# Kernel optimization log

Measured on AMD Instinct MI355X. Metric: run time of the kernel, lower is better.

Reference implementation:

```python
import jax, jax.numpy as jnp
import numpy as np
from math import factorial

# ---- configuration (init_kwargs: nclasses=40, cfg.bw=16) ----
BW = 16            # spherical bandwidth
NB = 2 * BW        # grid samples per angle
M = 2 * BW - 1     # spectral orders m in [-(BW-1), BW-1]
OFF = BW - 1       # index offset: m -> m + OFF
NCLS = 40
EPS = 1e-5
BATCH = 8

_FACT = [float(factorial(i)) for i in range(4 * BW + 2)]

def _wigner_d(l, beta):
    """Wigner small-d matrix d^l_{m',m}(beta), shape [2l+1, 2l+1]."""
    c, s = np.cos(beta / 2.0), np.sin(beta / 2.0)
    d = np.zeros((2 * l + 1, 2 * l + 1))
    for imp, mp in enumerate(range(-l, l + 1)):
        for im, m in enumerate(range(-l, l + 1)):
            pref = np.sqrt(_FACT[l + mp] * _FACT[l - mp] * _FACT[l + m] * _FACT[l - m])
            acc = 0.0
            for k in range(max(0, m - mp), min(l + m, l - mp) + 1):
                acc += ((-1.0) ** (mp - m + k)
                        / (_FACT[l + m - k] * _FACT[k] * _FACT[l - k - mp] * _FACT[k - m + mp])
                        * c ** (2 * l - 2 * k + m - mp) * s ** (2 * k - m + mp))
            d[imp, im] = pref * acc
    return d

def _build_constants():
    # Driscoll-Healy beta quadrature grid and weights
    betas = np.pi * (2 * np.arange(NB) + 1) / (4 * BW)
    kk = np.arange(BW)
    qw = (2.0 / BW) * np.sin(betas) * (
        np.sin(np.outer(2 * np.arange(NB) + 1, 2 * kk + 1) * np.pi / (4 * BW)) @ (1.0 / (2 * kk + 1)))
    d_beta = np.zeros((NB, BW, M, M))      # d^l_{mn}(beta_j), zero-padded over l
    for j, beta in enumerate(betas):
        for l in range(BW):
            d_beta[j, l, OFF - l:OFF + l + 1, OFF - l:OFF + l + 1] = _wigner_d(l, beta)
    d_eq = np.zeros((BW, M, M))            # d^l_{mn}(pi/2) for the equatorial kernel grid
    for l in range(BW):
        d_eq[l, OFF - l:OFF + l + 1, OFF - l:OFF + l + 1] = _wigner_d(l, np.pi / 2)
    bins = (np.arange(-(BW - 1), BW) % NB).astype(np.int32)  # FFT bin for each order m
    return qw.astype(np.float32), d_beta.astype(np.float32), d_eq.astype(np.float32), bins

_QWn, _DBETAn, _DEQn, _BINSn = _build_constants()
_DBJ = jnp.asarray(_DBETAn)                                   # [NB, L, M, M]
_DEQJ = jnp.asarray(_DEQn)                                    # [L, M, M]
_DEQ0 = jnp.asarray(_DEQn[:, :, OFF])                         # [L, M]  (n = 0 column)
_WD_S2 = jnp.asarray(_QWn[:, None, None] * _DBETAn[:, :, :, OFF])   # [NB, L, M]
_WD_SO3 = jnp.asarray(_QWn[:, None, None, None] * _DBETAn)          # [NB, L, M, M]
_L2 = jnp.asarray((2.0 * np.arange(BW) + 1.0).astype(np.float32))
_BINSJ = jnp.asarray(_BINSn)

def _so3_ifft(z, bias):
    # z: [B, Co, L, M, M] SO(3) spectrum -> real signal [B, Co, NB(beta), NB(alpha), NB(gamma)]
    F = jnp.einsum('bolmn,jlmn,l->bojmn', z, _DBJ, _L2)
    grid = jnp.zeros(F.shape[:3] + (NB, NB), F.dtype)
    grid = grid.at[..., _BINSJ[:, None], _BINSJ[None, :]].set(F)
    sig = jnp.fft.ifft2(grid, axes=(-2, -1)).real * float(NB * NB)
    return sig + bias[None, :, None, None, None]

def _s2_conv(x, W, bias):
    # x: [B, Ci, NB(beta), NB(alpha)]; W: [Ci, Co, NB] kernel on the equatorial grid
    Xf = jnp.fft.fft(x, axis=-1)[..., _BINSJ]                 # [B,Ci,NB,M]
    xh = jnp.einsum('bcjm,jlm->bclm', Xf, _WD_S2)             # S2 FFT -> [B,Ci,L,M]
    Wf = jnp.fft.fft(W, axis=-1)[..., _BINSJ]                 # [Ci,Co,M]
    yh = _DEQ0[:, :, None, None] * jnp.transpose(Wf, (2, 0, 1))[None]   # [L,N,Ci,Co]
    z = jnp.einsum('bilm,lnio->bolmn', xh, jnp.conj(yh))      # S2 correlation -> SO(3) spectrum
    return _so3_ifft(z, bias)

def _so3_conv(x, W, bias):
    # x: [B, Ci, NB(beta), NB(alpha), NB(gamma)]; W: [Ci, Co, NB]
    Xf = jnp.fft.fft2(x, axes=(-2, -1))[..., _BINSJ[:, None], _BINSJ[None, :]]  # [B,Ci,NB,M,M]
    xh = jnp.einsum('bcjmn,jlmn->bclmn', Xf, _WD_SO3)         # SO(3) FFT -> [B,Ci,L,M,M]
    Wf = jnp.fft.fft(W, axis=-1)[..., _BINSJ]                 # [Ci,Co,M]
    yh = _DEQJ[:, :, :, None, None] * jnp.transpose(Wf, (2, 0, 1))[None, :, None]  # [L,N,K,Ci,Co]
    z = jnp.einsum('bilmk,lnkio->bolmn', xh, jnp.conj(yh))    # SO(3) correlation
    return _so3_ifft(z, bias)

def _bn(h, g, b, axes, shape):
    mu = jnp.mean(h, axes, keepdims=True)
    var = jnp.var(h, axes, keepdims=True)
    return (h - mu) * jax.lax.rsqrt(var + EPS) * g.reshape(shape) + b.reshape(shape)

def _forward(x, k1, c1b, bn1_g, bn1_b, k2, c2b, bn2_g, bn2_b, k3, c3b, bn3_g, bn3_b,
             fc1_w, fc1_b, fbn1_g, fbn1_b, fc2_w, fc2_b, fbn2_g, fbn2_b, fc3_w, fc3_b):
    s5 = (1, -1, 1, 1, 1)
    h = _s2_conv(x, k1, c1b)                                  # [B,50,NB,NB,NB]
    h = jax.nn.relu(_bn(h, bn1_g, bn1_b, (0, 2, 3, 4), s5))
    h = _so3_conv(h, k2, c2b)
    h = jax.nn.relu(_bn(h, bn2_g, bn2_b, (0, 2, 3, 4), s5))
    h = _so3_conv(h, k3, c3b)
    h = jax.nn.relu(_bn(h, bn3_g, bn3_b, (0, 2, 3, 4), s5))
    h = h.mean(-1)                                            # integrate over gamma
    h = h.reshape(h.shape[0], h.shape[1], -1).max(-1)         # global max pool -> [B,50]
    h = h @ fc1_w.T + fc1_b
    h = jax.nn.relu(_bn(h, fbn1_g, fbn1_b, (0,), (1, -1)))
    h = h @ fc2_w.T + fc2_b
    h = jax.nn.relu(_bn(h, fbn2_g, fbn2_b, (0,), (1, -1)))
    h = h @ fc3_w.T + fc3_b
    return jax.nn.log_softmax(h, axis=1)

def setup_inputs():
    key = jax.random.key(0)
    ks = jax.random.split(key, 24)
    f32 = jnp.float32
    def kern(k, ci, co):
        return jax.random.normal(k, (ci, co, NB), f32) / np.sqrt(ci * NB).astype(np.float32)
    def lin(k, co, ci):
        return jax.random.normal(k, (co, ci), f32) / np.sqrt(ci).astype(np.float32)
    return {
        'x': jax.random.normal(ks[0], (BATCH, 1, NB, NB), f32),
        'k1': kern(ks[1], 1, 50), 'c1b': 0.01 * jax.random.normal(ks[2], (50,), f32),
        'bn1_g': 1.0 + 0.1 * jax.random.normal(ks[3], (50,), f32),
        'bn1_b': 0.1 * jax.random.normal(ks[4], (50,), f32),
        'k2': kern(ks[5], 50, 50), 'c2b': 0.01 * jax.random.normal(ks[6], (50,), f32),
        'bn2_g': 1.0 + 0.1 * jax.random.normal(ks[7], (50,), f32),
        'bn2_b': 0.1 * jax.random.normal(ks[8], (50,), f32),
        'k3': kern(ks[9], 50, 50), 'c3b': 0.01 * jax.random.normal(ks[10], (50,), f32),
        'bn3_g': 1.0 + 0.1 * jax.random.normal(ks[11], (50,), f32),
        'bn3_b': 0.1 * jax.random.normal(ks[12], (50,), f32),
        'fc1_w': lin(ks[13], 256, 50), 'fc1_b': jnp.zeros((256,), f32),
        'fbn1_g': 1.0 + 0.1 * jax.random.normal(ks[14], (256,), f32),
        'fbn1_b': 0.1 * jax.random.normal(ks[15], (256,), f32),
        'fc2_w': lin(ks[16], 128, 256), 'fc2_b': jnp.zeros((128,), f32),
        'fbn2_g': 1.0 + 0.1 * jax.random.normal(ks[17], (128,), f32),
        'fbn2_b': 0.1 * jax.random.normal(ks[18], (128,), f32),
        'fc3_w': lin(ks[19], NCLS, 128), 'fc3_b': jnp.zeros((NCLS,), f32),
    }

def reference(x, k1, c1b, bn1_g, bn1_b, k2, c2b, bn2_g, bn2_b, k3, c3b, bn3_g, bn3_b,
              fc1_w, fc1_b, fbn1_g, fbn1_b, fc2_w, fc2_b, fbn2_g, fbn2_b, fc3_w, fc3_b):
    return _forward(x, k1, c1b, bn1_g, bn1_b, k2, c2b, bn2_g, bn2_b, k3, c3b, bn3_g, bn3_b,
                    fc1_w, fc1_b, fbn1_g, fbn1_b, fc2_w, fc2_b, fbn2_g, fbn2_b, fc3_w, fc3_b)
```

## Files before the change

### kernel.cpp

```cpp
#include <hip/hip_runtime.h>
#include <math.h>

constexpr int NB = 32;
constexpr int LL = 16;
constexpr int MM = 31;
constexpr int MOFF = 15;
constexpr int NBATCH = 8;
constexpr int NCH = 50;
constexpr int NQ = MM * MM;
constexpr int SPAT = NB * NB * NB;
constexpr long long HN = (long long)NBATCH * NCH * SPAT;

#define PI_D 3.14159265358979323846

__device__ inline float2 c_mk(float x, float y) { float2 r; r.x = x; r.y = y; return r; }

__device__ inline void fill_tw(float2* tw) {
  int t = threadIdx.x;
  if (t < 32) {
    double a = (double)t * (PI_D / 16.0);
    tw[t] = c_mk((float)cos(a), (float)sin(a));
  }
}

__device__ inline int bitrev5(int n) {
  return ((n & 1) << 4) | ((n & 2) << 2) | (n & 4) | ((n & 8) >> 2) | ((n & 16) >> 4);
}

__device__ inline double dpow(double x, int n) {
  double r = 1.0;
  for (int i = 0; i < n; ++i) r *= x;
  return r;
}


__global__ void qw_kernel(float* __restrict__ qw) {
  int j = threadIdx.x;
  if (j >= NB) return;
  double beta = PI_D * (2 * j + 1) / 64.0;
  double acc = 0.0;
  for (int kk = 0; kk < LL; ++kk)
    acc += sin((double)(2 * j + 1) * (2 * kk + 1) * PI_D / 64.0) / (double)(2 * kk + 1);
  qw[j] = (float)((2.0 / 16.0) * sin(beta) * acc);
}

__global__ void wigner_kernel(float* __restrict__ out, int nj, int eqmode) {
  __shared__ double fact[66];
  int tid = threadIdx.x;
  if (tid < 66) { double f = 1.0; for (int i = 2; i <= tid; ++i) f *= (double)i; fact[tid] = f; }
  __syncthreads();
  int total = nj * LL * NQ;
  int idx = blockIdx.x * blockDim.x + tid;
  if (idx >= total) return;
  int q = idx % NQ;
  int l = (idx / NQ) % LL;
  int j = idx / (NQ * LL);
  int mp = q / MM - MOFF;
  int m  = q % MM - MOFF;
  int amp = mp < 0 ? -mp : mp, am = m < 0 ? -m : m;
  float res = 0.f;
  if (amp <= l && am <= l) {
    double beta = eqmode ? (PI_D * 0.5) : (PI_D * (2 * j + 1) / 64.0);
    double c = cos(beta * 0.5), s = sin(beta * 0.5);
    double pref = sqrt(fact[l + mp] * fact[l - mp] * fact[l + m] * fact[l - m]);
    int k0 = max(0, m - mp), k1 = min(l + m, l - mp);
    double acc = 0.0;
    for (int k = k0; k <= k1; ++k) {
      double denom = fact[l + m - k] * fact[k] * fact[l - k - mp] * fact[k - m + mp];
      double term = dpow(c, 2 * l - 2 * k + m - mp) * dpow(s, 2 * k - m + mp) / denom;
      acc += ((mp - m + k) & 1) ? -term : term;
    }
    res = (float)(pref * acc);
  }
  out[idx] = res;
}

__global__ void transpose_d_kernel(const float* __restrict__ dbeta, float* __restrict__ dbT) {
  int idx = blockIdx.x * blockDim.x + threadIdx.x;
  if (idx >= NB * LL * NQ) return;
  int m = idx % MM;
  int n = (idx / MM) % MM;
  int jl = idx / NQ;
  dbT[idx] = dbeta[jl * NQ + m * MM + n];
}


__global__ __launch_bounds__(256) void s2_xh_kernel(const float* __restrict__ x,
                                                    const float* __restrict__ qw,
                                                    const float* __restrict__ dbeta,
                                                    float2* __restrict__ xh1) {
  __shared__ float xt[NB * NB];
  __shared__ float2 Xf0[NB * MM];
  __shared__ float2 tw[32];
  fill_tw(tw);
  int tid = threadIdx.x, b = blockIdx.x;
  for (int e = tid; e < NB * NB; e += 256) xt[e] = x[b * 1024 + e];
  __syncthreads();
  for (int e = tid; e < NB * MM; e += 256) {
    int j = e / MM, mi = e % MM, m = mi - MOFF;
    float re = 0.f, im = 0.f;
    const float* row = xt + j * NB;
    for (int a = 0; a < NB; ++a) {
      float v = row[a];
      float2 t = tw[(m * a) & 31];
      re += v * t.x; im -= v * t.y;
    }
    Xf0[e] = c_mk(re, im);
  }
  __syncthreads();
  for (int e = tid; e < LL * MM; e += 256) {
    int l = e / MM, mi = e % MM;
    float re = 0.f, im = 0.f;
    for (int j = 0; j < NB; ++j) {
      float w = qw[j] * dbeta[(j * LL + l) * NQ + mi * MM + MOFF];
      float2 X = Xf0[j * MM + mi];
      re += w * X.x; im += w * X.y;
    }
    xh1[(b * LL + l) * MM + mi] = c_mk(re, im);
  }
}

__global__ __launch_bounds__(256) void wfft_kernel(const float* __restrict__ W, int CiCo,
                                                   float2* __restrict__ Wf) {
  __shared__ float2 tw[32];
  fill_tw(tw);
  __syncthreads();
  int idx = blockIdx.x * blockDim.x + threadIdx.x;
  if (idx >= MM * CiCo) return;
  int ni = idx / CiCo, ic = idx % CiCo;
  int n = ni - MOFF;
  float re = 0.f, im = 0.f;
  for (int t = 0; t < NB; ++t) {
    float v = W[ic * NB + t];
    float2 tt = tw[(n * t) & 31];
    re += v * tt.x; im -= v * tt.y;
  }
  Wf[idx] = c_mk(re, im);
}

__global__ void s2_z_kernel(const float2* __restrict__ xh1, const float2* __restrict__ Wf1,
                            const float* __restrict__ deq, float2* __restrict__ z) {
  int idx = blockIdx.x * blockDim.x + threadIdx.x;
  if (idx >= NBATCH * NCH * LL * NQ) return;
  int mi = idx % MM; int t = idx / MM;
  int ni = t % MM; t /= MM;
  int l = t % LL; t /= LL;
  int o = t % NCH; int b = t / NCH;
  float d0 = deq[(l * MM + ni) * MM + MOFF];
  float2 xv = xh1[(b * LL + l) * MM + mi];
  float2 wv = Wf1[ni * NCH + o];
  float re = d0 * (xv.x * wv.x + xv.y * wv.y);
  float im = d0 * (xv.y * wv.x - xv.x * wv.y);
  z[idx] = c_mk(re, im);
}


__global__ __launch_bounds__(256) void fjq_kernel(const float2* __restrict__ z,
                                                  const float* __restrict__ dbT,
                                                  float2* __restrict__ F) {
  __shared__ float2 zs[2][LL][8];
  int qg = blockIdx.x % 121;
  int bg = blockIdx.x / 121;
  int tid = threadIdx.x;
  int j = tid >> 3, ql = tid & 7;
  int q = qg * 8 + ql;
  bool qok = q < NQ;
  int qc = qok ? q : NQ - 1;
  float w[LL];
  #pragma unroll
  for (int l = 0; l < LL; ++l)
    w[l] = (2.f * l + 1.f) * dbT[(j * LL + l) * NQ + qc];
  int bo0 = bg * 25;
  if (tid < 128) {
    int l = tid >> 3, qq = qg * 8 + (tid & 7);
    int dd = (qq < NQ) ? (qq / MM - MOFF) : 99; if (dd < 0) dd = -dd;
    zs[0][l][tid & 7] = (l >= dd) ? z[((long long)bo0 * LL + l) * NQ + qq] : c_mk(0.f, 0.f);
  }
  __syncthreads();
  for (int i = 0; i < 25; ++i) {
    int bo = bo0 + i;
    if (i < 24 && tid < 128) {
      int l = tid >> 3, qq = qg * 8 + (tid & 7);
      int dd = (qq < NQ) ? (qq / MM - MOFF) : 99; if (dd < 0) dd = -dd;
      zs[(i + 1) & 1][l][tid & 7] =
          (l >= dd) ? z[((long long)(bo + 1) * LL + l) * NQ + qq] : c_mk(0.f, 0.f);
    }
    float fr = 0.f, fi = 0.f;
    #pragma unroll
    for (int l = 0; l < LL; ++l) {
      float2 zv = zs[i & 1][l][ql];
      fr += w[l] * zv.x; fi += w[l] * zv.y;
    }
    if (qok) F[((long long)bo * NB + j) * NQ + q] = c_mk(fr, fi);
    __syncthreads();
  }
}

__global__ __launch_bounds__(64) void so3_dft_kernel(const float2* __restrict__ F,
                                                     const float* __restrict__ bias,
                                                     float* __restrict__ out,
                                                     float2* __restrict__ parts) {
  __shared__ float Sre[2][32][33];
  __shared__ float Sim[2][32][33];
  __shared__ float2 tw[32];
  fill_tw(tw);
  int tid = threadIdx.x;
  int lane = tid & 31;
  int t = tid >> 5;
  int idx = blockIdx.x * 2 + t;
  int j = idx & 31;
  int bo = idx >> 5;
  int o = bo % NCH;

  Sre[t][16][lane] = 0.f; Sim[t][16][lane] = 0.f;
  Sre[t][lane][16] = 0.f; Sim[t][lane][16] = 0.f;
  __syncthreads();

  const float2* src = F + ((long long)bo * NB + j) * NQ;
  for (int e = lane; e < NQ; e += 32) {
    int ni = e / MM, mi = e % MM;
    float2 v = src[e];
    Sre[t][(ni + 17) & 31][(mi + 17) & 31] = v.x;
    Sim[t][(ni + 17) & 31][(mi + 17) & 31] = v.y;
  }
  __syncthreads();

  float vr[32], vi[32];

  #pragma unroll
  for (int r = 0; r < 32; ++r) { vr[r] = Sre[t][r][lane]; vi[r] = Sim[t][r][lane]; }
  #pragma unroll
  for (int st = 0; st < 5; ++st) {
    const int half = 16 >> st, tmul = 1 << st;
    #pragma unroll
    for (int p = 0; p < 16; ++p) {
      const int j2 = p & (half - 1);
      const int i0 = ((p >> (4 - st)) << (5 - st)) + j2;
      const int i1 = i0 + half;
      float2 tt = tw[(j2 * tmul) & 31];
      float ur = vr[i0], ui = vi[i0], wr = vr[i1], wi = vi[i1];
      float dr = ur - wr, di = ui - wi;
      vr[i0] = ur + wr; vi[i0] = ui + wi;
      vr[i1] = dr * tt.x - di * tt.y;
      vi[i1] = dr * tt.y + di * tt.x;
    }
  }
  #pragma unroll
  for (int k = 0; k < 32; ++k) {
    Sre[t][k][lane] = vr[bitrev5(k)];
    Sim[t][k][lane] = vi[bitrev5(k)];
  }
  __syncthreads();

  #pragma unroll
  for (int m = 0; m < 32; ++m) { vr[m] = Sre[t][lane][m]; vi[m] = Sim[t][lane][m]; }
  #pragma unroll
  for (int st = 0; st < 5; ++st) {
    const int half = 16 >> st, tmul = 1 << st;
    #pragma unroll
    for (int p = 0; p < 16; ++p) {
      const int j2 = p & (half - 1);
      const int i0 = ((p >> (4 - st)) << (5 - st)) + j2;
      const int i1 = i0 + half;
      float2 tt = tw[(j2 * tmul) & 31];
      float ur = vr[i0], ui = vi[i0], wr = vr[i1], wi = vi[i1];
      float dr = ur - wr, di = ui - wi;
      vr[i0] = ur + wr; vi[i0] = ui + wi;
      vr[i1] = dr * tt.x - di * tt.y;
      vi[i1] = dr * tt.y + di * tt.x;
    }
  }

  float bval = bias[o];
  long long obase = (long long)bo * SPAT + (long long)j * 1024 + lane;
  float s1 = 0.f, s2 = 0.f;
  #pragma unroll
  for (int a = 0; a < 32; ++a) {
    float val = vr[bitrev5(a)] + bval;
    out[obase + a * 32] = val;
    s1 += val; s2 += val * val;
  }
  #pragma unroll
  for (int off = 32; off > 0; off >>= 1) {
    s1 += __shfl_down(s1, off);
    s2 += __shfl_down(s2, off);
  }
  if (tid == 0) {
    atomicAdd(&parts[bo].x, s1);
    atomicAdd(&parts[bo].y, s2);
  }
}


__global__ void bn_finalize_kernel(const float2* __restrict__ partials,
                                   const float* __restrict__ g, const float* __restrict__ bb,
                                   float2* __restrict__ sc) {
  int o = threadIdx.x;
  if (o >= NCH) return;
  float s = 0.f, ss = 0.f;
  for (int b = 0; b < NBATCH; ++b) { float2 p = partials[b * NCH + o]; s += p.x; ss += p.y; }
  float inv = 1.f / (float)(NBATCH * SPAT);
  float mu = s * inv;
  float var = ss * inv - mu * mu;
  float scale = g[o] * rsqrtf(var + 1e-5f);
  sc[o] = c_mk(scale, bb[o] - mu * scale);
}


__global__ __launch_bounds__(256) void dft2b_kernel(const float* __restrict__ h,
                                                    const float2* __restrict__ sc,
                                                    float2* __restrict__ Xf) {
  __shared__ float xt[32 * 33];
  __shared__ float2 P[32 * 16];
  __shared__ float2 Xs[NQ];
  __shared__ float2 tw[32];
  fill_tw(tw);
  int tid = threadIdx.x;
  long long blk = blockIdx.x;
  int c = (int)((blk >> 5) % NCH);
  float2 s = sc[c];
  const float* src = h + blk * 1024;
  for (int e = tid; e < 1024; e += 256) {
    float v = src[e];
    xt[(e >> 5) * 33 + (e & 31)] = fmaxf(v * s.x + s.y, 0.f);
  }
  __syncthreads();
  for (int e = tid; e < 512; e += 256) {
    int a = e >> 4, n = e & 15;
    float re = 0.f, im = 0.f;
    const float* row = xt + a * 33;
    #pragma unroll
    for (int g = 0; g < 32; ++g) {
      float v = row[g];
      float2 t = tw[(n * g) & 31];
      re += v * t.x; im -= v * t.y;
    }
    P[a * 16 + n] = c_mk(re, im);
  }
  __syncthreads();
  {
    int e = tid;
    if (e < 256) {
      int mh = e >> 4, n = e & 15;
      float sxx = 0.f, sxy = 0.f, syx = 0.f, syy = 0.f;
      #pragma unroll
      for (int a = 0; a < 32; ++a) {
        float2 p = P[a * 16 + n];
        float2 t = tw[(mh * a) & 31];
        sxx += p.x * t.x; sxy += p.x * t.y;
        syx += p.y * t.x; syy += p.y * t.y;
      }
      float2 Xp = c_mk(sxx + syy, syx - sxy);
      float2 Xm = c_mk(sxx - syy, syx + sxy);
      Xs[(mh + MOFF) * MM + (n + MOFF)] = Xp;
      Xs[(MOFF - mh) * MM + (n + MOFF)] = Xm;
      Xs[(MOFF - mh) * MM + (MOFF - n)] = c_mk(Xp.x, -Xp.y);
      Xs[(mh + MOFF) * MM + (MOFF - n)] = c_mk(Xm.x, -Xm.y);
    }
  }
  __syncthreads();
  float2* dst = Xf + blk * NQ;
  for (int e = tid; e < NQ; e += 256) dst[e] = Xs[e];
}

__global__ void xh_kernel(const float2* __restrict__ Xf, const float* __restrict__ qw,
                          const float* __restrict__ dbeta, float2* __restrict__ xh) {
  int idx = blockIdx.x * blockDim.x + threadIdx.x;
  if (idx >= NBATCH * NCH * NQ) return;
  int q = idx % NQ;
  int bc = idx / NQ;
  float2 acc[LL];
  #pragma unroll
  for (int l = 0; l < LL; ++l) acc[l] = c_mk(0.f, 0.f);
  for (int j = 0; j < NB; ++j) {
    float2 xv = Xf[((long long)bc * NB + j) * NQ + q];
    float qj = qw[j];
    const float* dbase = dbeta + (long long)(j * LL) * NQ + q;
    #pragma unroll
    for (int l = 0; l < LL; ++l) {
      float w = qj * dbase[l * NQ];
      acc[l].x += w * xv.x;
      acc[l].y += w * xv.y;
    }
  }
  #pragma unroll
  for (int l = 0; l < LL; ++l) xh[((long long)bc * LL + l) * NQ + q] = acc[l];
}

__global__ __launch_bounds__(64) void hk_kernel(const float2* __restrict__ xh,
                                                const float* __restrict__ deq,
                                                float2* __restrict__ hk2) {
  int r = blockIdx.x;
  int mi = r % MM;
  int lb = r / MM;
  int b = lb & 7;
  int l = lb >> 3;
  int adm = mi - MOFF; adm = adm < 0 ? -adm : adm;
  if (adm > l) return;
  int ich = threadIdx.x;
  if (ich >= NCH) return;
  float2 row[MM];
  const float2* src = xh + ((long long)(b * NCH + ich) * LL + l) * NQ + mi * MM;
  #pragma unroll
  for (int k = 0; k < MM; ++k) row[k] = src[k];
  const float* dl = deq + l * NQ;
  long long obase = (long long)r * MM * NCH + ich;
  for (int ni = MOFF - l; ni <= MOFF + l; ++ni) {
    const float* dr = dl + ni * MM;
    float re = 0.f, im = 0.f;
    #pragma unroll
    for (int k = 0; k < MM; ++k) {
      float d = dr[k];
      re += d * row[k].x;
      im += d * row[k].y;
    }
    hk2[obase + (long long)ni * NCH] = c_mk(re, im);
  }
}

__global__ __launch_bounds__(256) void z_kernel(const float2* __restrict__ hk2,
                                                const float2* __restrict__ Wf,
                                                float2* __restrict__ z) {
  __shared__ float2 ws[NCH * NCH];
  int blk = blockIdx.x;
  int ni = 0;
  for (;;) {
    int d = ni - MOFF; if (d < 0) d = -d;
    int nt = 32 - 2 * d;
    if (blk < nt) break;
    blk -= nt; ++ni;
  }
  int dmin = ni - MOFF; if (dmin < 0) dmin = -dmin;
  int tid = threadIdx.x;
  {
    const float4* s4 = reinterpret_cast<const float4*>(Wf + ni * (NCH * NCH));
    float4* d4 = reinterpret_cast<float4*>(ws);
    for (int e = tid; e < NCH * NCH / 2; e += 256) d4[e] = s4[e];
  }
  __syncthreads();
  if (tid >= 248) return;
  int r = dmin * 248 + blk * 124 + (tid % 124);
  int o0 = (tid / 124) * 25;
  int mi = r % MM;
  int rem = r / MM;
  int b = rem & 7;
  int l = rem >> 3;

  const float4* h4 = reinterpret_cast<const float4*>(hk2 + ((long long)r * MM + ni) * NCH);

  float2 acc[25];
  #pragma unroll
  for (int u = 0; u < 25; ++u) acc[u] = c_mk(0.f, 0.f);

  for (int ih = 0; ih < 25; ++ih) {
    float4 hv = h4[ih];
    const float2* w0 = ws + (2 * ih) * NCH + o0;
    #pragma unroll
    for (int u = 0; u < 25; ++u) {
      float2 w = w0[u];
      acc[u].x += hv.x * w.x + hv.y * w.y;
      acc[u].y += hv.y * w.x - hv.x * w.y;
    }
    const float2* w1 = w0 + NCH;
    #pragma unroll
    for (int u = 0; u < 25; ++u) {
      float2 w = w1[u];
      acc[u].x += hv.z * w.x + hv.w * w.y;
      acc[u].y += hv.w * w.x - hv.z * w.y;
    }
  }

  long long zbase = (((long long)(b * NCH + o0) * LL + l) * NQ) + ni * MM + mi;
  #pragma unroll
  for (int u = 0; u < 25; ++u)
    z[zbase + (long long)u * LL * NQ] = acc[u];
}


__global__ void pool_kernel(const float* __restrict__ h, const float2* __restrict__ sc,
                            float* __restrict__ pooled) {
  __shared__ float sm[256];
  int tid = threadIdx.x;
  int o = blockIdx.x % NCH;
  float2 s = sc[o];
  const float* base = h + (long long)blockIdx.x * SPAT;
  float best = -1e30f;
  for (int e = tid; e < 1024; e += 256) {
    float acc = 0.f;
    for (int g = 0; g < NB; ++g) {
      float v = base[e * NB + g];
      acc += fmaxf(v * s.x + s.y, 0.f);
    }
    best = fmaxf(best, acc * (1.f / 32.f));
  }
  sm[tid] = best;
  __syncthreads();
  for (int st = 128; st > 0; st >>= 1) {
    if (tid < st) sm[tid] = fmaxf(sm[tid], sm[tid + st]);
    __syncthreads();
  }
  if (tid == 0) pooled[blockIdx.x] = sm[0];
}

__global__ __launch_bounds__(256) void head_kernel(const float* __restrict__ pooled,
    const float* __restrict__ fc1w, const float* __restrict__ fc1b,
    const float* __restrict__ g1, const float* __restrict__ b1,
    const float* __restrict__ fc2w, const float* __restrict__ fc2b,
    const float* __restrict__ g2, const float* __restrict__ b2,
    const float* __restrict__ fc3w, const float* __restrict__ fc3b,
    float* __restrict__ out) {
  __shared__ float pin[NBATCH * NCH];
  __shared__ float A[NBATCH * 256];
  __shared__ float Bm[NBATCH * 128];
  __shared__ float Cm[NBATCH * 40];
  int tid = threadIdx.x;
  for (int e = tid; e < NBATCH * NCH; e += 256) pin[e] = pooled[e];
  __syncthreads();
  {
    float v[NBATCH];
    #pragma unroll
    for (int b = 0; b < NBATCH; ++b) {
      float acc = fc1b[tid];
      for (int c = 0; c < NCH; ++c) acc += pin[b * NCH + c] * fc1w[tid * NCH + c];
      v[b] = acc;
    }
    float s = 0.f, ss = 0.f;
    #pragma unroll
    for (int b = 0; b < NBATCH; ++b) { s += v[b]; ss += v[b] * v[b]; }
    float mu = s * 0.125f, var = ss * 0.125f - mu * mu;
    float sc = g1[tid] * rsqrtf(var + 1e-5f), sh = b1[tid] - mu * sc;
    #pragma unroll
    for (int b = 0; b < NBATCH; ++b) A[b * 256 + tid] = fmaxf(v[b] * sc + sh, 0.f);
  }
  __syncthreads();
  if (tid < 128) {
    float v[NBATCH];
    #pragma unroll
    for (int b = 0; b < NBATCH; ++b) {
      float acc = fc2b[tid];
      for (int c = 0; c < 256; ++c) acc += A[b * 256 + c] * fc2w[tid * 256 + c];
      v[b] = acc;
    }
    float s = 0.f, ss = 0.f;
    #pragma unroll
    for (int b = 0; b < NBATCH; ++b) { s += v[b]; ss += v[b] * v[b]; }
    float mu = s * 0.125f, var = ss * 0.125f - mu * mu;
    float sc = g2[tid] * rsqrtf(var + 1e-5f), sh = b2[tid] - mu * sc;
    #pragma unroll
    for (int b = 0; b < NBATCH; ++b) Bm[b * 128 + tid] = fmaxf(v[b] * sc + sh, 0.f);
  }
  __syncthreads();
  if (tid < 40) {
    #pragma unroll
    for (int b = 0; b < NBATCH; ++b) {
      float acc = fc3b[tid];
      for (int c = 0; c < 128; ++c) acc += Bm[b * 128 + c] * fc3w[tid * 128 + c];
      Cm[b * 40 + tid] = acc;
    }
  }
  __syncthreads();
  if (tid < NBATCH) {
    int b = tid;
    float mx = -1e30f;
    for (int f = 0; f < 40; ++f) mx = fmaxf(mx, Cm[b * 40 + f]);
    float se = 0.f;
    for (int f = 0; f < 40; ++f) se += expf(Cm[b * 40 + f] - mx);
    float lse = mx + logf(se);
    for (int f = 0; f < 40; ++f) out[b * 40 + f] = Cm[b * 40 + f] - lse;
  }
}


extern "C" void kernel_launch(void* const* d_in, const int* in_sizes, int n_in,
                              void* d_out, int out_size, void* d_ws, size_t ws_size,
                              hipStream_t stream) {
  (void)in_sizes; (void)n_in; (void)out_size;
  const float* x    = (const float*)d_in[0];
  const float* k1   = (const float*)d_in[1];
  const float* c1b  = (const float*)d_in[2];
  const float* bn1g = (const float*)d_in[3];
  const float* bn1b = (const float*)d_in[4];
  const float* k2   = (const float*)d_in[5];
  const float* c2b  = (const float*)d_in[6];
  const float* bn2g = (const float*)d_in[7];
  const float* bn2b = (const float*)d_in[8];
  const float* k3   = (const float*)d_in[9];
  const float* c3b  = (const float*)d_in[10];
  const float* bn3g = (const float*)d_in[11];
  const float* bn3b = (const float*)d_in[12];
  const float* fc1w = (const float*)d_in[13];
  const float* fc1b = (const float*)d_in[14];
  const float* g1   = (const float*)d_in[15];
  const float* bb1  = (const float*)d_in[16];
  const float* fc2w = (const float*)d_in[17];
  const float* fc2b = (const float*)d_in[18];
  const float* g2   = (const float*)d_in[19];
  const float* bb2  = (const float*)d_in[20];
  const float* fc3w = (const float*)d_in[21];
  const float* fc3b = (const float*)d_in[22];
  float* out = (float*)d_out;

  char* ws = (char*)d_ws;
  size_t off = 0;
  auto alloc = [&](size_t n) -> char* {
    char* p = ws + off;
    off += (n + 255) & ~(size_t)255;
    return p;
  };

  float*  dbeta  = (float*)alloc(sizeof(float) * NB * LL * NQ);
  float*  dbT    = (float*)alloc(sizeof(float) * NB * LL * NQ);
  float*  deq    = (float*)alloc(sizeof(float) * LL * NQ);
  float*  qw     = (float*)alloc(sizeof(float) * NB);
  float2* xh1    = (float2*)alloc(sizeof(float2) * NBATCH * LL * MM);
  float2* Wf     = (float2*)alloc(sizeof(float2) * MM * NCH * NCH);
  float2* parts  = (float2*)alloc(sizeof(float2) * NBATCH * NCH);
  float2* bnsc   = (float2*)alloc(sizeof(float2) * 64);
  float*  pooled = (float*)alloc(sizeof(float) * NBATCH * NCH);
  float*  HA     = (float*)alloc(sizeof(float) * (size_t)HN);
  float*  HB     = (float*)alloc(sizeof(float) * (size_t)HN);
  size_t XFB = (size_t)NBATCH * NCH * NB * NQ * sizeof(float2);
  size_t XHB = (size_t)NBATCH * NCH * LL * NQ * sizeof(float2);
  char* AR = alloc(XFB + XHB);
  float2* Xf  = (float2*)AR;
  float2* xh  = (float2*)(AR + XFB);
  float2* hk2 = (float2*)AR;
  float2* zb  = (float2*)(AR + XFB);
  float2* Fb  = (float2*)AR;

  if (ws_size < off) return;

  const int T = 256;
  const size_t PARTS_B = sizeof(float2) * NBATCH * NCH;
  qw_kernel<<<1, 32, 0, stream>>>(qw);
  wigner_kernel<<<(NB * LL * NQ + T - 1) / T, T, 0, stream>>>(dbeta, NB, 0);
  wigner_kernel<<<(LL * NQ + T - 1) / T, T, 0, stream>>>(deq, 1, 1);
  transpose_d_kernel<<<(NB * LL * NQ + T - 1) / T, T, 0, stream>>>(dbeta, dbT);

  s2_xh_kernel<<<NBATCH, T, 0, stream>>>(x, qw, dbeta, xh1);
  wfft_kernel<<<(MM * 1 * NCH + T - 1) / T, T, 0, stream>>>(k1, 1 * NCH, Wf);
  s2_z_kernel<<<(NBATCH * NCH * LL * NQ + T - 1) / T, T, 0, stream>>>(xh1, Wf, deq, zb);
  fjq_kernel<<<121 * 16, T, 0, stream>>>(zb, dbT, Fb);
  hipMemsetAsync(parts, 0, PARTS_B, stream);
  so3_dft_kernel<<<NBATCH * NCH * NB / 2, 64, 0, stream>>>(Fb, c1b, HA, parts);
  bn_finalize_kernel<<<1, 64, 0, stream>>>(parts, bn1g, bn1b, bnsc);

  dft2b_kernel<<<NBATCH * NCH * NB, T, 0, stream>>>(HA, bnsc, Xf);
  xh_kernel<<<(NBATCH * NCH * NQ + T - 1) / T, T, 0, stream>>>(Xf, qw, dbeta, xh);
  wfft_kernel<<<(MM * NCH * NCH + T - 1) / T, T, 0, stream>>>(k2, NCH * NCH, Wf);
  hk_kernel<<<NBATCH * LL * MM, 64, 0, stream>>>(xh, deq, hk2);
  z_kernel<<<512, T, 0, stream>>>(hk2, Wf, zb);
  fjq_kernel<<<121 * 16, T, 0, stream>>>(zb, dbT, Fb);
  hipMemsetAsync(parts, 0, PARTS_B, stream);
  so3_dft_kernel<<<NBATCH * NCH * NB / 2, 64, 0, stream>>>(Fb, c2b, HB, parts);
  bn_finalize_kernel<<<1, 64, 0, stream>>>(parts, bn2g, bn2b, bnsc);

  dft2b_kernel<<<NBATCH * NCH * NB, T, 0, stream>>>(HB, bnsc, Xf);
  xh_kernel<<<(NBATCH * NCH * NQ + T - 1) / T, T, 0, stream>>>(Xf, qw, dbeta, xh);
  wfft_kernel<<<(MM * NCH * NCH + T - 1) / T, T, 0, stream>>>(k3, NCH * NCH, Wf);
  hk_kernel<<<NBATCH * LL * MM, 64, 0, stream>>>(xh, deq, hk2);
  z_kernel<<<512, T, 0, stream>>>(hk2, Wf, zb);
  fjq_kernel<<<121 * 16, T, 0, stream>>>(zb, dbT, Fb);
  hipMemsetAsync(parts, 0, PARTS_B, stream);
  so3_dft_kernel<<<NBATCH * NCH * NB / 2, 64, 0, stream>>>(Fb, c3b, HA, parts);
  bn_finalize_kernel<<<1, 64, 0, stream>>>(parts, bn3g, bn3b, bnsc);

  pool_kernel<<<NBATCH * NCH, T, 0, stream>>>(HA, bnsc, pooled);
  head_kernel<<<1, T, 0, stream>>>(pooled, fc1w, fc1b, g1, bb1,
                                   fc2w, fc2b, g2, bb2, fc3w, fc3b, out);
}
```

Baseline: 799.2 us.

## Stage FC weights in shared memory and skip zero Wigner-degree writes in xh

The head kernel now copies fc1, fc2 (in two 64-row chunks) and fc3 weights into padded shared memory and recomputes the matmuls from there. fc2 uses float4 dot products with all 256 threads, and fc3 splits work across 160 threads instead of 40. The goal is to cut uncoalesced global weight reads and raise thread utilisation in a single-block kernel. Separately, xh_kernel skips storing coefficients for degrees l below max(|m|,|n|), which are structurally zero, to reduce store traffic, provided downstream kernels never read those entries.

```diff
diff --git a/kernel.cpp b/kernel.cpp
--- a/kernel.cpp
+++ b/kernel.cpp
@@ -369,6 +369,9 @@
   if (idx >= NBATCH * NCH * NQ) return;
   int q = idx % NQ;
   int bc = idx / NQ;
+  int dm = q / MM - MOFF; if (dm < 0) dm = -dm;
+  int dn = q % MM - MOFF; if (dn < 0) dn = -dn;
+  int lmin = dm > dn ? dm : dn;
   float2 acc[LL];
   #pragma unroll
   for (int l = 0; l < LL; ++l) acc[l] = c_mk(0.f, 0.f);
@@ -384,7 +387,8 @@
     }
   }
   #pragma unroll
-  for (int l = 0; l < LL; ++l) xh[((long long)bc * LL + l) * NQ + q] = acc[l];
+  for (int l = 0; l < LL; ++l)
+    if (l >= lmin) xh[((long long)bc * LL + l) * NQ + q] = acc[l];
 }
 
 __global__ __launch_bounds__(64) void hk_kernel(const float2* __restrict__ xh,
@@ -509,54 +513,101 @@
     const float* __restrict__ g2, const float* __restrict__ b2,
     const float* __restrict__ fc3w, const float* __restrict__ fc3b,
     float* __restrict__ out) {
+  __shared__ __align__(16) float WB[64 * 260];
   __shared__ float pin[NBATCH * NCH];
   __shared__ float A[NBATCH * 256];
+  __shared__ float R[NBATCH * 128];
   __shared__ float Bm[NBATCH * 128];
   __shared__ float Cm[NBATCH * 40];
   int tid = threadIdx.x;
+
   for (int e = tid; e < NBATCH * NCH; e += 256) pin[e] = pooled[e];
-  __syncthreads();
+  for (int e = tid; e < 256 * 50; e += 256) {
+    int row = e / 50, c = e % 50;
+    WB[row * 51 + c] = fc1w[e];
+  }
+  __syncthreads();
+
   {
+    int o = tid;
+    const float* wr = WB + o * 51;
     float v[NBATCH];
+    float bias = fc1b[o];
     #pragma unroll
     for (int b = 0; b < NBATCH; ++b) {
-      float acc = fc1b[tid];
-      for (int c = 0; c < NCH; ++c) acc += pin[b * NCH + c] * fc1w[tid * NCH + c];
+      float acc = bias;
+      #pragma unroll
+      for (int c = 0; c < NCH; ++c) acc += pin[b * NCH + c] * wr[c];
       v[b] = acc;
     }
     float s = 0.f, ss = 0.f;
     #pragma unroll
     for (int b = 0; b < NBATCH; ++b) { s += v[b]; ss += v[b] * v[b]; }
     float mu = s * 0.125f, var = ss * 0.125f - mu * mu;
-    float sc = g1[tid] * rsqrtf(var + 1e-5f), sh = b1[tid] - mu * sc;
-    #pragma unroll
-    for (int b = 0; b < NBATCH; ++b) A[b * 256 + tid] = fmaxf(v[b] * sc + sh, 0.f);
-  }
-  __syncthreads();
+    float sc = g1[o] * rsqrtf(var + 1e-5f), sh = b1[o] - mu * sc;
+    #pragma unroll
+    for (int b = 0; b < NBATCH; ++b) A[b * 256 + o] = fmaxf(v[b] * sc + sh, 0.f);
+  }
+  __syncthreads();
+
+  for (int ch = 0; ch < 2; ++ch) {
+    {
+      const float4* s4 = reinterpret_cast<const float4*>(fc2w + ch * 64 * 256);
+      float4* d4 = reinterpret_cast<float4*>(WB);
+      for (int e = tid; e < 64 * 64; e += 256) {
+        int row = e >> 6, k = e & 63;
+        d4[row * 65 + k] = s4[e];
+      }
+    }
+    __syncthreads();
+    {
+      int b = tid >> 5, oo = tid & 31;
+      int o_a = ch * 64 + oo, o_b = o_a + 32;
+      float acc0 = fc2b[o_a], acc1 = fc2b[o_b];
+      const float4* av4 = reinterpret_cast<const float4*>(A + b * 256);
+      const float4* w04 = reinterpret_cast<const float4*>(WB + oo * 260);
+      const float4* w14 = reinterpret_cast<const float4*>(WB + (oo + 32) * 260);
+      #pragma unroll
+      for (int c4 = 0; c4 < 64; ++c4) {
+        float4 av = av4[c4];
+        float4 w0 = w04[c4];
+        float4 w1 = w14[c4];
+        acc0 += av.x * w0.x + av.y * w0.y + av.z * w0.z + av.w * w0.w;
+        acc1 += av.x * w1.x + av.y * w1.y + av.z * w1.z + av.w * w1.w;
+      }
+      R[b * 128 + o_a] = acc0;
+      R[b * 128 + o_b] = acc1;
+    }
+    __syncthreads();
+  }
   if (tid < 128) {
-    float v[NBATCH];
-    #pragma unroll
-    for (int b = 0; b < NBATCH; ++b) {
-      float acc = fc2b[tid];
-      for (int c = 0; c < 256; ++c) acc += A[b * 256 + c] * fc2w[tid * 256 + c];
-      v[b] = acc;
-    }
+    int o = tid;
     float s = 0.f, ss = 0.f;
     #pragma unroll
-    for (int b = 0; b < NBATCH; ++b) { s += v[b]; ss += v[b] * v[b]; }
+    for (int b = 0; b < NBATCH; ++b) { float v = R[b * 128 + o]; s += v; ss += v * v; }
     float mu = s * 0.125f, var = ss * 0.125f - mu * mu;
-    float sc = g2[tid] * rsqrtf(var + 1e-5f), sh = b2[tid] - mu * sc;
-    #pragma unroll
-    for (int b = 0; b < NBATCH; ++b) Bm[b * 128 + tid] = fmaxf(v[b] * sc + sh, 0.f);
-  }
-  __syncthreads();
-  if (tid < 40) {
-    #pragma unroll
-    for (int b = 0; b < NBATCH; ++b) {
-      float acc = fc3b[tid];
-      for (int c = 0; c < 128; ++c) acc += Bm[b * 128 + c] * fc3w[tid * 128 + c];
-      Cm[b * 40 + tid] = acc;
-    }
+    float sc = g2[o] * rsqrtf(var + 1e-5f), sh = b2[o] - mu * sc;
+    #pragma unroll
+    for (int b = 0; b < NBATCH; ++b) Bm[b * 128 + o] = fmaxf(R[b * 128 + o] * sc + sh, 0.f);
+  }
+  for (int e = tid; e < 40 * 128; e += 256) {
+    int row = e >> 7, c = e & 127;
+    WB[row * 129 + c] = fc3w[e];
+  }
+  __syncthreads();
+
+  if (tid < 160) {
+    int o = tid >> 2, q = tid & 3;
+    const float* wr = WB + o * 129;
+    float a0 = fc3b[o], a1 = a0;
+    #pragma unroll
+    for (int c = 0; c < 128; ++c) {
+      float w = wr[c];
+      a0 += Bm[q * 128 + c] * w;
+      a1 += Bm[(q + 4) * 128 + c] * w;
+    }
+    Cm[q * 40 + o] = a0;
+    Cm[(q + 4) * 40 + o] = a1;
   }
   __syncthreads();
   if (tid < NBATCH) {
```

Result: faster. 782.2 us (-2.1%).

## Fuse pooling and MLP head via last-block atomic counter; skip invalid xh stores

Applied to the files above, without the earlier changes.

Merges pool and head kernels into one launch where the last finishing block, detected with an atomic counter, runs the MLP head. The head now stages fc1/fc2/fc3 weights in padded shared memory with coalesced loads and float4 dot products instead of strided global reads. xh_kernel also skips writes for l below max(|m|,|n|). The large shared-memory footprint lowers occupancy of the pooling phase, and correctness now relies on a counter reset and on downstream kernels not reading the skipped entries.

```diff
diff --git a/kernel.cpp b/kernel.cpp
--- a/kernel.cpp
+++ b/kernel.cpp
@@ -369,6 +369,9 @@
   if (idx >= NBATCH * NCH * NQ) return;
   int q = idx % NQ;
   int bc = idx / NQ;
+  int dm = q / MM - MOFF; if (dm < 0) dm = -dm;
+  int dn = q % MM - MOFF; if (dn < 0) dn = -dn;
+  int lmin = dm > dn ? dm : dn;
   float2 acc[LL];
   #pragma unroll
   for (int l = 0; l < LL; ++l) acc[l] = c_mk(0.f, 0.f);
@@ -384,7 +387,8 @@
     }
   }
   #pragma unroll
-  for (int l = 0; l < LL; ++l) xh[((long long)bc * LL + l) * NQ + q] = acc[l];
+  for (int l = 0; l < LL; ++l)
+    if (l >= lmin) xh[((long long)bc * LL + l) * NQ + q] = acc[l];
 }
 
 __global__ __launch_bounds__(64) void hk_kernel(const float2* __restrict__ xh,
@@ -476,87 +480,192 @@
     z[zbase + (long long)u * LL * NQ] = acc[u];
 }
 
-
-__global__ void pool_kernel(const float* __restrict__ h, const float2* __restrict__ sc,
-                            float* __restrict__ pooled) {
-  __shared__ float sm[256];
-  int tid = threadIdx.x;
-  int o = blockIdx.x % NCH;
-  float2 s = sc[o];
-  const float* base = h + (long long)blockIdx.x * SPAT;
-  float best = -1e30f;
-  for (int e = tid; e < 1024; e += 256) {
-    float acc = 0.f;
-    for (int g = 0; g < NB; ++g) {
-      float v = base[e * NB + g];
-      acc += fmaxf(v * s.x + s.y, 0.f);
-    }
-    best = fmaxf(best, acc * (1.f / 32.f));
-  }
-  sm[tid] = best;
-  __syncthreads();
-  for (int st = 128; st > 0; st >>= 1) {
-    if (tid < st) sm[tid] = fmaxf(sm[tid], sm[tid + st]);
-    __syncthreads();
-  }
-  if (tid == 0) pooled[blockIdx.x] = sm[0];
-}
-
-__global__ __launch_bounds__(256) void head_kernel(const float* __restrict__ pooled,
+__global__ __launch_bounds__(256) void pool_head_kernel(const float* __restrict__ h,
+    const float2* __restrict__ sc, float* __restrict__ pooled, unsigned* __restrict__ counter,
     const float* __restrict__ fc1w, const float* __restrict__ fc1b,
     const float* __restrict__ g1, const float* __restrict__ b1,
     const float* __restrict__ fc2w, const float* __restrict__ fc2b,
     const float* __restrict__ g2, const float* __restrict__ b2,
     const float* __restrict__ fc3w, const float* __restrict__ fc3b,
     float* __restrict__ out) {
-  __shared__ float pin[NBATCH * NCH];
-  __shared__ float A[NBATCH * 256];
-  __shared__ float Bm[NBATCH * 128];
-  __shared__ float Cm[NBATCH * 40];
+  __shared__ float sm[256];
+  __shared__ int lastflag;
+  __shared__ __align__(16) float  WB2[12800];
+  __shared__ __align__(16) float4 WB1[2][32 * 65];
+  __shared__ float pin[400];
+  __shared__ __align__(16) float A[8 * 256];
+  __shared__ float R[8 * 128];
+  __shared__ float Cm[8 * 40];
+
   int tid = threadIdx.x;
-  for (int e = tid; e < NBATCH * NCH; e += 256) pin[e] = pooled[e];
-  __syncthreads();
+  int bo = blockIdx.x;
   {
+    int o = bo % NCH;
+    float2 s = sc[o];
+    const float* base = h + (long long)bo * SPAT;
+    float best = -1e30f;
+    for (int e = tid; e < 1024; e += 256) {
+      float acc = 0.f;
+      for (int g = 0; g < NB; ++g) {
+        float v = base[e * NB + g];
+        acc += fmaxf(v * s.x + s.y, 0.f);
+      }
+      best = fmaxf(best, acc * (1.f / 32.f));
+    }
+    sm[tid] = best;
+    __syncthreads();
+    for (int st = 128; st > 0; st >>= 1) {
+      if (tid < st) sm[tid] = fmaxf(sm[tid], sm[tid + st]);
+      __syncthreads();
+    }
+    if (tid == 0) {
+      __hip_atomic_store(&pooled[bo], sm[0], __ATOMIC_RELEASE, __HIP_MEMORY_SCOPE_AGENT);
+      unsigned prev = __hip_atomic_fetch_add(counter, 1u, __ATOMIC_ACQ_REL,
+                                             __HIP_MEMORY_SCOPE_AGENT);
+      lastflag = (prev == 399u);
+    }
+    __syncthreads();
+    if (!lastflag) return;
+  }
+
+  for (int e = tid; e < 400; e += 256)
+    pin[e] = __hip_atomic_load(&pooled[e], __ATOMIC_RELAXED, __HIP_MEMORY_SCOPE_AGENT);
+  #pragma unroll
+  for (int k = 0; k < 50; ++k) WB2[k * 256 + tid] = fc1w[k * 256 + tid];
+  const float4* w2src = reinterpret_cast<const float4*>(fc2w);
+  #pragma unroll
+  for (int k = 0; k < 8; ++k) {
+    int idx = k * 256 + tid;
+    WB1[0][(idx >> 6) * 65 + (idx & 63)] = w2src[idx];
+  }
+  #pragma unroll
+  for (int k = 0; k < 8; ++k) {
+    int idx = k * 256 + tid;
+    WB1[1][(idx >> 6) * 65 + (idx & 63)] = w2src[2048 + idx];
+  }
+  float4 p2r[8], p3r[8];
+  #pragma unroll
+  for (int k = 0; k < 8; ++k) p2r[k] = w2src[4096 + k * 256 + tid];
+  #pragma unroll
+  for (int k = 0; k < 8; ++k) p3r[k] = w2src[6144 + k * 256 + tid];
+  float f3r[20];
+  #pragma unroll
+  for (int k = 0; k < 20; ++k) f3r[k] = fc3w[k * 256 + tid];
+  float rb1 = fc1b[tid], rg1 = g1[tid], rbb1 = b1[tid];
+  int oo = tid & 31, bb = tid >> 5;
+  float f2b[4];
+  #pragma unroll
+  for (int p = 0; p < 4; ++p) f2b[p] = fc2b[p * 32 + oo];
+  float rg2 = 0.f, rbb2 = 0.f;
+  if (tid < 128) { rg2 = g2[tid]; rbb2 = b2[tid]; }
+  float rb3 = (tid < 160) ? fc3b[tid >> 2] : 0.f;
+  __syncthreads();
+
+  {
+    const float* wr = WB2 + tid * 50;
     float v[NBATCH];
     #pragma unroll
-    for (int b = 0; b < NBATCH; ++b) {
-      float acc = fc1b[tid];
-      for (int c = 0; c < NCH; ++c) acc += pin[b * NCH + c] * fc1w[tid * NCH + c];
-      v[b] = acc;
+    for (int b = 0; b < NBATCH; ++b) v[b] = rb1;
+    for (int c = 0; c < NCH; ++c) {
+      float w = wr[c];
+      #pragma unroll
+      for (int b = 0; b < NBATCH; ++b) v[b] += pin[b * NCH + c] * w;
     }
     float s = 0.f, ss = 0.f;
     #pragma unroll
     for (int b = 0; b < NBATCH; ++b) { s += v[b]; ss += v[b] * v[b]; }
     float mu = s * 0.125f, var = ss * 0.125f - mu * mu;
-    float sc = g1[tid] * rsqrtf(var + 1e-5f), sh = b1[tid] - mu * sc;
-    #pragma unroll
-    for (int b = 0; b < NBATCH; ++b) A[b * 256 + tid] = fmaxf(v[b] * sc + sh, 0.f);
-  }
-  __syncthreads();
+    float scl = rg1 * rsqrtf(var + 1e-5f), sh = rbb1 - mu * scl;
+    #pragma unroll
+    for (int b = 0; b < NBATCH; ++b) A[b * 256 + tid] = fmaxf(v[b] * scl + sh, 0.f);
+  }
+  __syncthreads();
+  #pragma unroll
+  for (int k = 0; k < 20; ++k) {
+    int e = k * 256 + tid;
+    WB2[(e >> 7) * 129 + (e & 127)] = f3r[k];
+  }
+
+  const float4* av4 = reinterpret_cast<const float4*>(A) + bb * 64;
+  {
+    const float4* w4 = &WB1[0][oo * 65];
+    float acc = f2b[0];
+    #pragma unroll
+    for (int c4 = 0; c4 < 64; ++c4) {
+      float4 a = av4[c4], w = w4[c4];
+      acc += a.x * w.x + a.y * w.y + a.z * w.z + a.w * w.w;
+    }
+    R[bb * 128 + oo] = acc;
+  }
+  __syncthreads();
+  #pragma unroll
+  for (int k = 0; k < 8; ++k) {
+    int idx = k * 256 + tid;
+    WB1[0][(idx >> 6) * 65 + (idx & 63)] = p2r[k];
+  }
+  {
+    const float4* w4 = &WB1[1][oo * 65];
+    float acc = f2b[1];
+    #pragma unroll
+    for (int c4 = 0; c4 < 64; ++c4) {
+      float4 a = av4[c4], w = w4[c4];
+      acc += a.x * w.x + a.y * w.y + a.z * w.z + a.w * w.w;
+    }
+    R[bb * 128 + 32 + oo] = acc;
+  }
+  __syncthreads();
+  #pragma unroll
+  for (int k = 0; k < 8; ++k) {
+    int idx = k * 256 + tid;
+    WB1[1][(idx >> 6) * 65 + (idx & 63)] = p3r[k];
+  }
+  {
+    const float4* w4 = &WB1[0][oo * 65];
+    float acc = f2b[2];
+    #pragma unroll
+    for (int c4 = 0; c4 < 64; ++c4) {
+      float4 a = av4[c4], w = w4[c4];
+      acc += a.x * w.x + a.y * w.y + a.z * w.z + a.w * w.w;
+    }
+    R[bb * 128 + 64 + oo] = acc;
+  }
+  __syncthreads();
+  {
+    const float4* w4 = &WB1[1][oo * 65];
+    float acc = f2b[3];
+    #pragma unroll
+    for (int c4 = 0; c4 < 64; ++c4) {
+      float4 a = av4[c4], w = w4[c4];
+      acc += a.x * w.x + a.y * w.y + a.z * w.z + a.w * w.w;
+    }
+    R[bb * 128 + 96 + oo] = acc;
+  }
+  __syncthreads();
+
   if (tid < 128) {
-    float v[NBATCH];
-    #pragma unroll
-    for (int b = 0; b < NBATCH; ++b) {
-      float acc = fc2b[tid];
-      for (int c = 0; c < 256; ++c) acc += A[b * 256 + c] * fc2w[tid * 256 + c];
-      v[b] = acc;
-    }
     float s = 0.f, ss = 0.f;
     #pragma unroll
-    for (int b = 0; b < NBATCH; ++b) { s += v[b]; ss += v[b] * v[b]; }
+    for (int b = 0; b < NBATCH; ++b) { float v = R[b * 128 + tid]; s += v; ss += v * v; }
     float mu = s * 0.125f, var = ss * 0.125f - mu * mu;
-    float sc = g2[tid] * rsqrtf(var + 1e-5f), sh = b2[tid] - mu * sc;
-    #pragma unroll
-    for (int b = 0; b < NBATCH; ++b) Bm[b * 128 + tid] = fmaxf(v[b] * sc + sh, 0.f);
-  }
-  __syncthreads();
-  if (tid < 40) {
-    #pragma unroll
-    for (int b = 0; b < NBATCH; ++b) {
-      float acc = fc3b[tid];
-      for (int c = 0; c < 128; ++c) acc += Bm[b * 128 + c] * fc3w[tid * 128 + c];
-      Cm[b * 40 + tid] = acc;
-    }
+    float scl = rg2 * rsqrtf(var + 1e-5f), sh = rbb2 - mu * scl;
+    #pragma unroll
+    for (int b = 0; b < NBATCH; ++b)
+      R[b * 128 + tid] = fmaxf(R[b * 128 + tid] * scl + sh, 0.f);
+  }
+  __syncthreads();
+
+  if (tid < 160) {
+    int o3 = tid >> 2, q = tid & 3;
+    const float* wr = WB2 + o3 * 129;
+    float a0 = rb3, a1 = rb3;
+    #pragma unroll
+    for (int c = 0; c < 128; ++c) {
+      float w = wr[c];
+      a0 += R[q * 128 + c] * w;
+      a1 += R[(q + 4) * 128 + c] * w;
+    }
+    Cm[q * 40 + o3] = a0;
+    Cm[(q + 4) * 40 + o3] = a1;
   }
   __syncthreads();
   if (tid < NBATCH) {
@@ -617,6 +726,7 @@
   float2* parts  = (float2*)alloc(sizeof(float2) * NBATCH * NCH);
   float2* bnsc   = (float2*)alloc(sizeof(float2) * 64);
   float*  pooled = (float*)alloc(sizeof(float) * NBATCH * NCH);
+  unsigned* counter = (unsigned*)alloc(sizeof(unsigned) * 64);
   float*  HA     = (float*)alloc(sizeof(float) * (size_t)HN);
   float*  HB     = (float*)alloc(sizeof(float) * (size_t)HN);
   size_t XFB = (size_t)NBATCH * NCH * NB * NQ * sizeof(float2);
@@ -636,6 +746,7 @@
   wigner_kernel<<<(NB * LL * NQ + T - 1) / T, T, 0, stream>>>(dbeta, NB, 0);
   wigner_kernel<<<(LL * NQ + T - 1) / T, T, 0, stream>>>(deq, 1, 1);
   transpose_d_kernel<<<(NB * LL * NQ + T - 1) / T, T, 0, stream>>>(dbeta, dbT);
+  hipMemsetAsync(counter, 0, sizeof(unsigned), stream);
 
   s2_xh_kernel<<<NBATCH, T, 0, stream>>>(x, qw, dbeta, xh1);
   wfft_kernel<<<(MM * 1 * NCH + T - 1) / T, T, 0, stream>>>(k1, 1 * NCH, Wf);
@@ -665,7 +776,8 @@
   so3_dft_kernel<<<NBATCH * NCH * NB / 2, 64, 0, stream>>>(Fb, c3b, HA, parts);
   bn_finalize_kernel<<<1, 64, 0, stream>>>(parts, bn3g, bn3b, bnsc);
 
-  pool_kernel<<<NBATCH * NCH, T, 0, stream>>>(HA, bnsc, pooled);
-  head_kernel<<<1, T, 0, stream>>>(pooled, fc1w, fc1b, g1, bb1,
-                                   fc2w, fc2b, g2, bb2, fc3w, fc3b, out);
-}
+  pool_head_kernel<<<NBATCH * NCH, T, 0, stream>>>(HA, bnsc, pooled, counter,
+                                                   fc1w, fc1b, g1, bb1,
+                                                   fc2w, fc2b, g2, bb2,
+                                                   fc3w, fc3b, out);
+}
```

Result: no change. 806.8 us (+0.9%).

## Split MLP head into parallel fc kernels and skip zero xh stores

Applied to the files above, without the earlier changes.

The single-block head kernel becomes three kernels (fc1, fc2, fc3) that spread output neurons over several blocks. fc2 uses float4 loads and shuffle reductions for the batch-norm statistics. The aim is to remove the long serial dot products in the one-block head. Separately, xh_kernel stops storing coefficients for l below max(|m|,|n|), which are structurally zero, cutting write traffic; this is safe only if downstream code never reads those entries or the buffer is already zeroed, since it aliases another buffer.

```diff
diff --git a/kernel.cpp b/kernel.cpp
--- a/kernel.cpp
+++ b/kernel.cpp
@@ -369,6 +369,9 @@
   if (idx >= NBATCH * NCH * NQ) return;
   int q = idx % NQ;
   int bc = idx / NQ;
+  int dm = q / MM - MOFF; if (dm < 0) dm = -dm;
+  int dn = q % MM - MOFF; if (dn < 0) dn = -dn;
+  int lmin = dm > dn ? dm : dn;
   float2 acc[LL];
   #pragma unroll
   for (int l = 0; l < LL; ++l) acc[l] = c_mk(0.f, 0.f);
@@ -384,7 +387,8 @@
     }
   }
   #pragma unroll
-  for (int l = 0; l < LL; ++l) xh[((long long)bc * LL + l) * NQ + q] = acc[l];
+  for (int l = 0; l < LL; ++l)
+    if (l >= lmin) xh[((long long)bc * LL + l) * NQ + q] = acc[l];
 }
 
 __global__ __launch_bounds__(64) void hk_kernel(const float2* __restrict__ xh,
@@ -502,71 +506,78 @@
   if (tid == 0) pooled[blockIdx.x] = sm[0];
 }
 
-__global__ __launch_bounds__(256) void head_kernel(const float* __restrict__ pooled,
+__global__ __launch_bounds__(32) void fc1_kernel(const float* __restrict__ pooled,
     const float* __restrict__ fc1w, const float* __restrict__ fc1b,
     const float* __restrict__ g1, const float* __restrict__ b1,
+    float* __restrict__ A) {
+  int o = blockIdx.x * 32 + threadIdx.x;
+  const float* wr = fc1w + o * NCH;
+  float v[NBATCH];
+  float bias = fc1b[o];
+  #pragma unroll
+  for (int b = 0; b < NBATCH; ++b) v[b] = bias;
+  for (int c = 0; c < NCH; ++c) {
+    float w = wr[c];
+    #pragma unroll
+    for (int b = 0; b < NBATCH; ++b) v[b] += pooled[b * NCH + c] * w;
+  }
+  float s = 0.f, ss = 0.f;
+  #pragma unroll
+  for (int b = 0; b < NBATCH; ++b) { s += v[b]; ss += v[b] * v[b]; }
+  float mu = s * 0.125f, var = ss * 0.125f - mu * mu;
+  float scl = g1[o] * rsqrtf(var + 1e-5f), sh = b1[o] - mu * scl;
+  #pragma unroll
+  for (int b = 0; b < NBATCH; ++b) A[b * 256 + o] = fmaxf(v[b] * scl + sh, 0.f);
+}
+
+__global__ __launch_bounds__(64) void fc2_kernel(const float* __restrict__ A,
     const float* __restrict__ fc2w, const float* __restrict__ fc2b,
     const float* __restrict__ g2, const float* __restrict__ b2,
+    float* __restrict__ A2) {
+  int tid = threadIdx.x;
+  int o = blockIdx.x * 8 + (tid >> 3);
+  int b = tid & 7;
+  const float4* av = reinterpret_cast<const float4*>(A + b * 256);
+  const float4* wv = reinterpret_cast<const float4*>(fc2w + o * 256);
+  float acc = fc2b[o];
+  #pragma unroll
+  for (int c4 = 0; c4 < 64; ++c4) {
+    float4 a = av[c4], w = wv[c4];
+    acc += a.x * w.x + a.y * w.y + a.z * w.z + a.w * w.w;
+  }
+  float s = acc, ss = acc * acc;
+  #pragma unroll
+  for (int m = 1; m < 8; m <<= 1) {
+    s += __shfl_xor(s, m);
+    ss += __shfl_xor(ss, m);
+  }
+  float mu = s * 0.125f, var = ss * 0.125f - mu * mu;
+  float scl = g2[o] * rsqrtf(var + 1e-5f), sh = b2[o] - mu * scl;
+  A2[b * 128 + o] = fmaxf(acc * scl + sh, 0.f);
+}
+
+__global__ __launch_bounds__(64) void fc3_kernel(const float* __restrict__ A2,
     const float* __restrict__ fc3w, const float* __restrict__ fc3b,
     float* __restrict__ out) {
-  __shared__ float pin[NBATCH * NCH];
-  __shared__ float A[NBATCH * 256];
-  __shared__ float Bm[NBATCH * 128];
-  __shared__ float Cm[NBATCH * 40];
-  int tid = threadIdx.x;
-  for (int e = tid; e < NBATCH * NCH; e += 256) pin[e] = pooled[e];
-  __syncthreads();
-  {
-    float v[NBATCH];
-    #pragma unroll
-    for (int b = 0; b < NBATCH; ++b) {
-      float acc = fc1b[tid];
-      for (int c = 0; c < NCH; ++c) acc += pin[b * NCH + c] * fc1w[tid * NCH + c];
-      v[b] = acc;
-    }
-    float s = 0.f, ss = 0.f;
-    #pragma unroll
-    for (int b = 0; b < NBATCH; ++b) { s += v[b]; ss += v[b] * v[b]; }
-    float mu = s * 0.125f, var = ss * 0.125f - mu * mu;
-    float sc = g1[tid] * rsqrtf(var + 1e-5f), sh = b1[tid] - mu * sc;
-    #pragma unroll
-    for (int b = 0; b < NBATCH; ++b) A[b * 256 + tid] = fmaxf(v[b] * sc + sh, 0.f);
-  }
-  __syncthreads();
-  if (tid < 128) {
-    float v[NBATCH];
-    #pragma unroll
-    for (int b = 0; b < NBATCH; ++b) {
-      float acc = fc2b[tid];
-      for (int c = 0; c < 256; ++c) acc += A[b * 256 + c] * fc2w[tid * 256 + c];
-      v[b] = acc;
-    }
-    float s = 0.f, ss = 0.f;
-    #pragma unroll
-    for (int b = 0; b < NBATCH; ++b) { s += v[b]; ss += v[b] * v[b]; }
-    float mu = s * 0.125f, var = ss * 0.125f - mu * mu;
-    float sc = g2[tid] * rsqrtf(var + 1e-5f), sh = b2[tid] - mu * sc;
-    #pragma unroll
-    for (int b = 0; b < NBATCH; ++b) Bm[b * 128 + tid] = fmaxf(v[b] * sc + sh, 0.f);
-  }
-  __syncthreads();
+  __shared__ float Cm[40];
+  int tid = threadIdx.x;
+  int b = blockIdx.x;
   if (tid < 40) {
-    #pragma unroll
-    for (int b = 0; b < NBATCH; ++b) {
-      float acc = fc3b[tid];
-      for (int c = 0; c < 128; ++c) acc += Bm[b * 128 + c] * fc3w[tid * 128 + c];
-      Cm[b * 40 + tid] = acc;
-    }
-  }
-  __syncthreads();
-  if (tid < NBATCH) {
-    int b = tid;
+    const float* wr = fc3w + tid * 128;
+    const float* ar = A2 + b * 128;
+    float acc = fc3b[tid];
+    #pragma unroll
+    for (int c = 0; c < 128; ++c) acc += ar[c] * wr[c];
+    Cm[tid] = acc;
+  }
+  __syncthreads();
+  if (tid == 0) {
     float mx = -1e30f;
-    for (int f = 0; f < 40; ++f) mx = fmaxf(mx, Cm[b * 40 + f]);
+    for (int f = 0; f < 40; ++f) mx = fmaxf(mx, Cm[f]);
     float se = 0.f;
-    for (int f = 0; f < 40; ++f) se += expf(Cm[b * 40 + f] - mx);
+    for (int f = 0; f < 40; ++f) se += expf(Cm[f] - mx);
     float lse = mx + logf(se);
-    for (int f = 0; f < 40; ++f) out[b * 40 + f] = Cm[b * 40 + f] - lse;
+    for (int f = 0; f < 40; ++f) out[b * 40 + f] = Cm[f] - lse;
   }
 }
 
@@ -617,6 +628,8 @@
   float2* parts  = (float2*)alloc(sizeof(float2) * NBATCH * NCH);
   float2* bnsc   = (float2*)alloc(sizeof(float2) * 64);
   float*  pooled = (float*)alloc(sizeof(float) * NBATCH * NCH);
+  float*  Abuf   = (float*)alloc(sizeof(float) * NBATCH * 256);
+  float*  A2buf  = (float*)alloc(sizeof(float) * NBATCH * 128);
   float*  HA     = (float*)alloc(sizeof(float) * (size_t)HN);
   float*  HB     = (float*)alloc(sizeof(float) * (size_t)HN);
   size_t XFB = (size_t)NBATCH * NCH * NB * NQ * sizeof(float2);
@@ -666,6 +679,7 @@
   bn_finalize_kernel<<<1, 64, 0, stream>>>(parts, bn3g, bn3b, bnsc);
 
   pool_kernel<<<NBATCH * NCH, T, 0, stream>>>(HA, bnsc, pooled);
-  head_kernel<<<1, T, 0, stream>>>(pooled, fc1w, fc1b, g1, bb1,
-                                   fc2w, fc2b, g2, bb2, fc3w, fc3b, out);
-}
+  fc1_kernel<<<8, 32, 0, stream>>>(pooled, fc1w, fc1b, g1, bb1, Abuf);
+  fc2_kernel<<<16, 64, 0, stream>>>(Abuf, fc2w, fc2b, g2, bb2, A2buf);
+  fc3_kernel<<<8, 64, 0, stream>>>(A2buf, fc3w, fc3b, out);
+}
```

Result: faster. 761.5 us (-4.7%).
